# Kernel optimization log

Measured on AMD Instinct MI355X. Metric: run time of the kernel, lower is better.

## Reference

```python
import jax, jax.numpy as jnp
import numpy as np

B, N, E = 2, 2048, 1024
H, D = 16, 64  # context_dim = H*D = 1024


def setup_inputs() -> dict:
    key = jax.random.key(0)
    ks = jax.random.split(key, 6)
    s = 0.02
    return {
        "input_emb": jax.random.normal(ks[0], (B, N, E), dtype=jnp.float32),
        "Wq": jax.random.normal(ks[1], (E, H * D), dtype=jnp.float32) * s,
        "Wk": jax.random.normal(ks[2], (E, D), dtype=jnp.float32) * s,
        "Wv": jax.random.normal(ks[3], (E, D), dtype=jnp.float32) * s,
        "Wo": jax.random.normal(ks[4], (H * D, H * D), dtype=jnp.float32) * s,
        "bo": jax.random.normal(ks[5], (H * D,), dtype=jnp.float32) * s,
    }


def reference(input_emb, Wq, Wk, Wv, Wo, bo):
    b, n, _ = input_emb.shape
    Q = (input_emb @ Wq).reshape(b, n, H, D)          # (B,N,H,D)
    K = input_emb @ Wk                                 # (B,N,D) shared across heads (MQA)
    V = input_emb @ Wv                                 # (B,N,D)
    # scores: (B,H,N,N); mask is applied before scaling in the torch code,
    # but -inf/scale == -inf so mask-then-scale == scale-then-mask.
    scores = jnp.einsum("bnhd,bmd->bhnm", Q, K) / jnp.sqrt(jnp.float32(D))
    causal = jnp.tril(jnp.ones((n, n), dtype=bool))    # True = keep
    scores = jnp.where(causal[None, None], scores, -jnp.inf)
    weights = jax.nn.softmax(scores, axis=-1)          # dropout rate 0.0 -> identity
    Z = jnp.einsum("bhnm,bmd->bnhd", weights, V).reshape(b, n, H * D)
    return Z @ Wo + bo
```

## Files before the change

kernel.cpp:

```cpp
#include <hip/hip_runtime.h>
#include <hip/hip_bf16.h>


#define NQ 2048
#define BATCH 2
#define HEADS 16
#define HD 64
#define EMB 1024
#define NKV 1152

typedef short s16x8 __attribute__((ext_vector_type(8)));
typedef float f32x4 __attribute__((ext_vector_type(4)));
typedef unsigned int u32x4 __attribute__((ext_vector_type(4)));
typedef unsigned short ushort_t;

__device__ __forceinline__ ushort_t f2bf(float f) {
    unsigned u = __builtin_bit_cast(unsigned, f);
    u += 0x7fff + ((u >> 16) & 1);
    return (ushort_t)(u >> 16);
}

__device__ __forceinline__ void store_out(float* p, float v) { *p = v; }
__device__ __forceinline__ void store_out(ushort_t* p, float v) { *p = f2bf(v); }

#define GL16(g, l)                                                                  \
    __builtin_amdgcn_global_load_lds(                                               \
        (const __attribute__((address_space(1))) unsigned int*)(g),                 \
        (__attribute__((address_space(3))) unsigned int*)(l), 16, 0, 0)

__global__ __launch_bounds__(256) void prep(const float* __restrict__ x,
                                            const float* __restrict__ Wq,
                                            const float* __restrict__ Wk,
                                            const float* __restrict__ Wv,
                                            const float* __restrict__ Wo,
                                            ushort_t* __restrict__ xb,
                                            ushort_t* __restrict__ Wqkv_t,
                                            ushort_t* __restrict__ Wo_t) {
    const int bid = blockIdx.x, t = threadIdx.x;
    if (bid < 4096) {
        const int i = bid * 1024 + t * 4;
        const float4 v = *(const float4*)&x[i];
        ushort_t o[4] = {f2bf(v.x), f2bf(v.y), f2bf(v.z), f2bf(v.w)};
        *(uint2*)&xb[i] = *(uint2*)o;
        return;
    }
    int tb = bid - 4096;
    const float* src; ushort_t* dst; int N, n0, k0;
    if (tb < 1024)      { src = Wq; N = 1024; dst = Wqkv_t;
                          n0 = (tb & 31) * 32; k0 = (tb >> 5) * 32; }
    else if (tb < 1088) { tb -= 1024; src = Wk; N = 64; dst = Wqkv_t + (size_t)1024 * EMB;
                          n0 = (tb & 1) * 32; k0 = (tb >> 1) * 32; }
    else if (tb < 1152) { tb -= 1088; src = Wv; N = 64; dst = Wqkv_t + (size_t)1088 * EMB;
                          n0 = (tb & 1) * 32; k0 = (tb >> 1) * 32; }
    else                { tb -= 1152; src = Wo; N = 1024; dst = Wo_t;
                          n0 = (tb & 31) * 32; k0 = (tb >> 5) * 32; }
    __shared__ float tile[32][33];
    const int tx = t & 31, ty = t >> 5;
#pragma unroll
    for (int i = 0; i < 32; i += 8)
        tile[ty + i][tx] = src[(size_t)(k0 + ty + i) * N + n0 + tx];
    __syncthreads();
#pragma unroll
    for (int i = 0; i < 32; i += 8)
        dst[(size_t)(n0 + ty + i) * EMB + k0 + tx] = f2bf(tile[tx][ty + i]);
}

template<bool HAS_BIAS, bool WRITE_VT, typename OutT>
__global__ __launch_bounds__(256) void gemm_bf16(const ushort_t* __restrict__ A,
                                                 const ushort_t* __restrict__ Bt,
                                                 const float* __restrict__ bias,
                                                 OutT* __restrict__ C,
                                                 ushort_t* __restrict__ Vt,
                                                 int M, int N, int K) {
    __shared__ __align__(16) ushort_t Al[64 * 32];
    __shared__ __align__(16) ushort_t Bl[128 * 32];
    const int t = threadIdx.x;
    const int w = t >> 6, lane = t & 63, quad = lane >> 4, ln = lane & 15;
    const int row0 = blockIdx.y * 64, col0 = blockIdx.x * 128;

    const int rA = t >> 2;
    const int lcA = (t & 3) ^ ((rA >> 1) & 3);
    const int rB1 = 64 + rA;
    const ushort_t* ga  = A  + (size_t)(row0 + rA) * K + lcA * 8;
    const ushort_t* gb0 = Bt + (size_t)(col0 + rA) * K + lcA * 8;
    const ushort_t* gb1 = Bt + (size_t)(col0 + rB1) * K + lcA * 8;
    ushort_t* lA  = Al + w * 512;
    ushort_t* lB0 = Bl + w * 512;
    ushort_t* lB1 = Bl + 2048 + w * 512;

    f32x4 acc[4][2] = {};
    const int sw = (ln >> 1) & 3;
    for (int k0 = 0; k0 < K; k0 += 32) {
        GL16(ga, lA); GL16(gb0, lB0); GL16(gb1, lB1);
        ga += 32; gb0 += 32; gb1 += 32;
        __syncthreads();

        s16x8 af[4], bf[2];
#pragma unroll
        for (int mt = 0; mt < 4; ++mt)
            af[mt] = *(const s16x8*)&Al[(mt * 16 + ln) * 32 + ((quad ^ sw) * 8)];
#pragma unroll
        for (int nt = 0; nt < 2; ++nt)
            bf[nt] = *(const s16x8*)&Bl[(w * 32 + nt * 16 + ln) * 32 + ((quad ^ sw) * 8)];
#pragma unroll
        for (int mt = 0; mt < 4; ++mt)
#pragma unroll
            for (int nt = 0; nt < 2; ++nt)
                acc[mt][nt] = __builtin_amdgcn_mfma_f32_16x16x32_bf16(
                    af[mt], bf[nt], acc[mt][nt], 0, 0, 0);
        __syncthreads();
    }

#pragma unroll
    for (int nt = 0; nt < 2; ++nt) {
        const int col = col0 + w * 32 + nt * 16 + ln;
        const float bv = HAS_BIAS ? bias[col] : 0.f;
#pragma unroll
        for (int mt = 0; mt < 4; ++mt) {
#pragma unroll
            for (int r = 0; r < 4; ++r) {
                const int row = row0 + mt * 16 + quad * 4 + r;
                float v = acc[mt][nt][r] + bv;
                if (WRITE_VT && col < 1024) v *= 0.18033688011112043f;
                store_out(&C[(size_t)row * N + col], v);
            }
            if (WRITE_VT && col >= 1088) {
                const int d = col - 1088;
                const int n = row0 + mt * 16 + quad * 4;
                const int bb = n >> 11, nn = n & 2047;
                ushort_t tmp[4] = {f2bf(acc[mt][nt][0]), f2bf(acc[mt][nt][1]),
                                   f2bf(acc[mt][nt][2]), f2bf(acc[mt][nt][3])};
                *(uint2*)&Vt[((size_t)bb * 64 + d) * NQ + nn] = *(uint2*)tmp;
            }
        }
    }
}

__device__ __forceinline__ void stage_tile(ushort_t* lds, const ushort_t* g,
                                           size_t rstride, int w, int lane) {
#pragma unroll
    for (int it = 0; it < 2; ++it) {
        const int u = (w * 2 + it) * 64 + lane;
        const int row = u >> 3, pc = u & 7;
        const int lc = pc ^ (row & 7);
        GL16(g + (size_t)row * rstride + lc * 8, lds + (size_t)(w * 2 + it) * 512);
    }
}

__device__ __forceinline__ void stage_k(ushort_t* lds, const ushort_t* g,
                                        int w, int lane) {
#pragma unroll
    for (int it = 0; it < 2; ++it) {
        const int u = (w * 2 + it) * 64 + lane;
        const int row = u >> 3, pc = u & 7;
        const int lc = pc ^ (row & 7);
        const int grow = (row & 32) | (((row >> 2) & 3) << 3) |
                         (((row >> 4) & 1) << 2) | (row & 3);
        GL16(g + (size_t)grow * NKV + lc * 8, lds + (size_t)(w * 2 + it) * 512);
    }
}

__device__ __forceinline__ s16x8 frag(const ushort_t* lds, int row, int lc) {
    const int phys = lc ^ (row & 7);
    return *(const s16x8*)&lds[row * 64 + phys * 8];
}

__global__ __launch_bounds__(256, 4) void attn_mfma(const ushort_t* __restrict__ QKV,
                                                    const ushort_t* __restrict__ Vt,
                                                    ushort_t* __restrict__ Z) {
    const int bid = blockIdx.x;
    const int b = (bid >> 4) & 1, h = bid & 15;
    const int i = bid >> 5, k = i >> 3, j = i & 7;
    const int qt = (k == 0) ? 2 * j : (k == 1) ? 31 - 2 * j
                 : (k == 2) ? 2 * j + 1 : 30 - 2 * j;
    const int t = threadIdx.x;
    const int w = t >> 6, lane = t & 63, quad = lane >> 4, ln = lane & 15;

    __shared__ __align__(16) ushort_t Kl[2][64 * 64];
    __shared__ __align__(16) ushort_t Vl[2][64 * 64];

    const ushort_t* Kg = QKV + (size_t)b * NQ * NKV + 1024;
    const ushort_t* Vg = Vt + (size_t)b * 64 * NQ;

    const ushort_t* Qg = QKV + (size_t)(b * NQ + qt * 64 + w * 16 + ln) * NKV + h * HD;
    const s16x8 aQ0 = *(const s16x8*)(Qg + quad * 8);
    const s16x8 aQ1 = *(const s16x8*)(Qg + 32 + quad * 8);

    stage_k(Kl[0], Kg, w, lane);
    stage_tile(Vl[0], Vg, NQ, w, lane);
    __syncthreads();

    f32x4 o[4];
#pragma unroll
    for (int ii = 0; ii < 4; ++ii) o[ii] = f32x4{0.f, 0.f, 0.f, 0.f};
    float mrow = -1e30f, lrow = 0.f;
    const int qrel = w * 16 + ln;

#pragma unroll 1
    for (int jt = 0; jt <= qt; ++jt) {
        const int cur = jt & 1;
        if (jt < qt) {
            stage_k(Kl[cur ^ 1], Kg + (size_t)(jt + 1) * 64 * NKV, w, lane);
            stage_tile(Vl[cur ^ 1], Vg + (jt + 1) * 64, NQ, w, lane);
        }
        const ushort_t* Kc = Kl[cur];
        const ushort_t* Vc = Vl[cur];

        f32x4 s[4];
        __builtin_amdgcn_s_setprio(1);
#pragma unroll
        for (int nt = 0; nt < 4; ++nt) {
            f32x4 acc = f32x4{0.f, 0.f, 0.f, 0.f};
            acc = __builtin_amdgcn_mfma_f32_16x16x32_bf16(
                frag(Kc, nt * 16 + ln, quad), aQ0, acc, 0, 0, 0);
            acc = __builtin_amdgcn_mfma_f32_16x16x32_bf16(
                frag(Kc, nt * 16 + ln, 4 + quad), aQ1, acc, 0, 0, 0);
            s[nt] = acc;
        }
        __builtin_amdgcn_s_setprio(0);

        if (jt == qt) {
#pragma unroll
            for (int nt = 0; nt < 4; ++nt)
#pragma unroll
                for (int r = 0; r < 4; ++r) {
                    const int kv = (nt >> 1) * 32 + quad * 8 + (nt & 1) * 4 + r;
                    if (kv > qrel) s[nt][r] = -1e30f;
                }
        }

        float m0 = fmaxf(fmaxf(s[0][0], s[0][1]), fmaxf(s[0][2], s[0][3]));
        float m1 = fmaxf(fmaxf(s[1][0], s[1][1]), fmaxf(s[1][2], s[1][3]));
        float m2 = fmaxf(fmaxf(s[2][0], s[2][1]), fmaxf(s[2][2], s[2][3]));
        float m3 = fmaxf(fmaxf(s[3][0], s[3][1]), fmaxf(s[3][2], s[3][3]));
        float rmax = fmaxf(fmaxf(m0, m1), fmaxf(m2, m3));
        rmax = fmaxf(rmax, __shfl_xor(rmax, 16));
        rmax = fmaxf(rmax, __shfl_xor(rmax, 32));

        if (!__all(rmax - mrow <= 8.f)) {
            const float mnew = fmaxf(mrow, rmax);
            const float al = __builtin_amdgcn_exp2f(mrow - mnew);
            mrow = mnew;
            lrow *= al;
#pragma unroll
            for (int ntd = 0; ntd < 4; ++ntd)
#pragma unroll
                for (int r = 0; r < 4; ++r) o[ntd][r] *= al;
        }

        float rsum = 0.f;
#pragma unroll
        for (int nt = 0; nt < 4; ++nt)
#pragma unroll
            for (int r = 0; r < 4; ++r) {
                const float pv = __builtin_amdgcn_exp2f(s[nt][r] - mrow);
                s[nt][r] = pv;
                rsum += pv;
            }
        rsum += __shfl_xor(rsum, 16);
        rsum += __shfl_xor(rsum, 32);
        lrow += rsum;

        unsigned pw0[4], pw1[4];
#pragma unroll
        for (int jj = 0; jj < 4; ++jj) {
            const int nt0 = jj >> 1, rr = 2 * (jj & 1);
            asm("v_cvt_pk_bf16_f32 %0, %1, %2"
                : "=v"(pw0[jj]) : "v"(s[nt0][rr]), "v"(s[nt0][rr + 1]));
            asm("v_cvt_pk_bf16_f32 %0, %1, %2"
                : "=v"(pw1[jj]) : "v"(s[2 + nt0][rr]), "v"(s[2 + nt0][rr + 1]));
        }
        const u32x4 q0 = {pw0[0], pw0[1], pw0[2], pw0[3]};
        const u32x4 q1 = {pw1[0], pw1[1], pw1[2], pw1[3]};
        const s16x8 bP0 = __builtin_bit_cast(s16x8, q0);
        const s16x8 bP1 = __builtin_bit_cast(s16x8, q1);

        __builtin_amdgcn_s_setprio(1);
#pragma unroll
        for (int ntd = 0; ntd < 4; ++ntd) {
            o[ntd] = __builtin_amdgcn_mfma_f32_16x16x32_bf16(
                frag(Vc, ntd * 16 + ln, quad), bP0, o[ntd], 0, 0, 0);
            o[ntd] = __builtin_amdgcn_mfma_f32_16x16x32_bf16(
                frag(Vc, ntd * 16 + ln, 4 + quad), bP1, o[ntd], 0, 0, 0);
        }
        __builtin_amdgcn_s_setprio(0);
        __syncthreads();
    }

    const float invl = 1.f / lrow;
    const size_t row = (size_t)(b * NQ + qt * 64 + w * 16 + ln);
#pragma unroll
    for (int ntd = 0; ntd < 4; ++ntd) {
        ushort_t tmp[4];
#pragma unroll
        for (int r = 0; r < 4; ++r) tmp[r] = f2bf(o[ntd][r] * invl);
        *(uint2*)&Z[row * EMB + h * HD + ntd * 16 + quad * 4] = *(uint2*)tmp;
    }
}

extern "C" void kernel_launch(void* const* d_in, const int* in_sizes, int n_in,
                              void* d_out, int out_size, void* d_ws, size_t ws_size,
                              hipStream_t stream) {
    const float* x  = (const float*)d_in[0];
    const float* Wq = (const float*)d_in[1];
    const float* Wk = (const float*)d_in[2];
    const float* Wv = (const float*)d_in[3];
    const float* Wo = (const float*)d_in[4];
    const float* bo = (const float*)d_in[5];
    float* out = (float*)d_out;

    const int M = BATCH * NQ;
    char* ws = (char*)d_ws;
    ushort_t* xb     = (ushort_t*)ws;
    ushort_t* Wqkv_t = (ushort_t*)(ws + (size_t)8  * 1024 * 1024);
    ushort_t* Wo_t   = (ushort_t*)(ws + (size_t)11 * 1024 * 1024);
    ushort_t* QKV    = (ushort_t*)(ws + (size_t)13 * 1024 * 1024);
    ushort_t* Vt     = (ushort_t*)(ws + (size_t)23 * 1024 * 1024);
    ushort_t* Zb     = (ushort_t*)(ws + (size_t)24 * 1024 * 1024);

    dim3 blk(256);
    prep<<<dim3(6272), blk, 0, stream>>>(x, Wq, Wk, Wv, Wo, xb, Wqkv_t, Wo_t);
    gemm_bf16<false, true, ushort_t><<<dim3(NKV / 128, M / 64), blk, 0, stream>>>(
        xb, Wqkv_t, nullptr, QKV, Vt, M, NKV, EMB);
    attn_mfma<<<dim3(1024), blk, 0, stream>>>(QKV, Vt, Zb);
    gemm_bf16<true, false, float><<<dim3(EMB / 128, M / 64), blk, 0, stream>>>(
        Zb, Wo_t, bo, out, nullptr, M, EMB, EMB);
}
```

Before: 166.5 us.

## Enlarge GEMM tiles to 128x128x64 with double-buffered LDS and block swizzle

Reworks the bf16 GEMM used for the QKV and output projections. Tiles grow from 64x128 with K-step 32 to 128x128 with K-step 64, and each wave now computes a 64x64 sub-tile. LDS is double-buffered so the global loads for the next K-step are issued before the current step's MFMAs, and the block index is remapped so neighbouring blocks are spread across the grid. The intent is more data reuse per load, fewer barriers per unit of work, and overlap of memory traffic with compute. In exchange it uses 64KB of LDS and more registers per block, and launches half as many blocks (288 and 256), which may underfill the GPU's compute units.

```diff
diff --git a/kernel.cpp b/kernel.cpp
--- a/kernel.cpp
+++ b/kernel.cpp
@@ -65,68 +65,105 @@
         dst[(size_t)(n0 + ty + i) * EMB + k0 + tx] = f2bf(tile[tx][ty + i]);
 }
 
+__device__ __forceinline__ s16x8 frag(const ushort_t* lds, int row, int lc) {
+    const int phys = lc ^ (row & 7);
+    return *(const s16x8*)&lds[row * 64 + phys * 8];
+}
+
 template<bool HAS_BIAS, bool WRITE_VT, typename OutT>
-__global__ __launch_bounds__(256) void gemm_bf16(const ushort_t* __restrict__ A,
-                                                 const ushort_t* __restrict__ Bt,
-                                                 const float* __restrict__ bias,
-                                                 OutT* __restrict__ C,
-                                                 ushort_t* __restrict__ Vt,
-                                                 int M, int N, int K) {
-    __shared__ __align__(16) ushort_t Al[64 * 32];
-    __shared__ __align__(16) ushort_t Bl[128 * 32];
+__global__ __launch_bounds__(256, 2) void gemm_bf16(const ushort_t* __restrict__ A,
+                                                    const ushort_t* __restrict__ Bt,
+                                                    const float* __restrict__ bias,
+                                                    OutT* __restrict__ C,
+                                                    ushort_t* __restrict__ Vt,
+                                                    int M, int N, int K) {
+    __shared__ __align__(16) ushort_t Al[2][128 * 64];
+    __shared__ __align__(16) ushort_t Bl[2][128 * 64];
     const int t = threadIdx.x;
     const int w = t >> 6, lane = t & 63, quad = lane >> 4, ln = lane & 15;
-    const int row0 = blockIdx.y * 64, col0 = blockIdx.x * 128;
-
-    const int rA = t >> 2;
-    const int lcA = (t & 3) ^ ((rA >> 1) & 3);
-    const int rB1 = 64 + rA;
-    const ushort_t* ga  = A  + (size_t)(row0 + rA) * K + lcA * 8;
-    const ushort_t* gb0 = Bt + (size_t)(col0 + rA) * K + lcA * 8;
-    const ushort_t* gb1 = Bt + (size_t)(col0 + rB1) * K + lcA * 8;
-    ushort_t* lA  = Al + w * 512;
-    ushort_t* lB0 = Bl + w * 512;
-    ushort_t* lB1 = Bl + 2048 + w * 512;
-
-    f32x4 acc[4][2] = {};
-    const int sw = (ln >> 1) & 3;
-    for (int k0 = 0; k0 < K; k0 += 32) {
-        GL16(ga, lA); GL16(gb0, lB0); GL16(gb1, lB1);
-        ga += 32; gb0 += 32; gb1 += 32;
+    const int wm = w >> 1, wn = w & 1;
+
+    const int nwg = gridDim.x * gridDim.y;
+    int lin = blockIdx.y * gridDim.x + blockIdx.x;
+    lin = (lin & 7) * (nwg >> 3) + (lin >> 3);
+    const int bx = lin % gridDim.x, by = lin / gridDim.x;
+    const int row0 = by * 128, col0 = bx * 128;
+
+    const ushort_t* pA[4];
+    const ushort_t* pB[4];
+#pragma unroll
+    for (int it = 0; it < 4; ++it) {
+        const int u = (w * 4 + it) * 64 + lane;
+        const int row = u >> 3, pc = u & 7;
+        const int lc = pc ^ (row & 7);
+        pA[it] = A + (size_t)(row0 + row) * K + lc * 8;
+        pB[it] = Bt + (size_t)(col0 + row) * K + lc * 8;
+    }
+
+#define STAGE_AB(la, lb)                                                            \
+    {                                                                               \
+        _Pragma("unroll")                                                           \
+        for (int it = 0; it < 4; ++it) {                                            \
+            GL16(pA[it], (la) + (w * 4 + it) * 512);                                \
+            GL16(pB[it], (lb) + (w * 4 + it) * 512);                                \
+            pA[it] += 64;                                                           \
+            pB[it] += 64;                                                           \
+        }                                                                           \
+    }
+
+    f32x4 acc[4][4] = {};
+    const int nk = K >> 6;
+
+    STAGE_AB(Al[0], Bl[0]);
+    __syncthreads();
+
+#pragma unroll 1
+    for (int ks = 0; ks < nk; ++ks) {
+        const int cur = ks & 1;
+        if (ks + 1 < nk) STAGE_AB(Al[cur ^ 1], Bl[cur ^ 1]);
+
+        const ushort_t* la = Al[cur];
+        const ushort_t* lb = Bl[cur];
+        s16x8 af[4][2], bf[4][2];
+#pragma unroll
+        for (int mt = 0; mt < 4; ++mt) {
+            af[mt][0] = frag(la, wm * 64 + mt * 16 + ln, quad);
+            af[mt][1] = frag(la, wm * 64 + mt * 16 + ln, 4 + quad);
+        }
+#pragma unroll
+        for (int nt = 0; nt < 4; ++nt) {
+            bf[nt][0] = frag(lb, wn * 64 + nt * 16 + ln, quad);
+            bf[nt][1] = frag(lb, wn * 64 + nt * 16 + ln, 4 + quad);
+        }
+#pragma unroll
+        for (int mt = 0; mt < 4; ++mt)
+#pragma unroll
+            for (int nt = 0; nt < 4; ++nt) {
+                acc[mt][nt] = __builtin_amdgcn_mfma_f32_16x16x32_bf16(
+                    af[mt][0], bf[nt][0], acc[mt][nt], 0, 0, 0);
+                acc[mt][nt] = __builtin_amdgcn_mfma_f32_16x16x32_bf16(
+                    af[mt][1], bf[nt][1], acc[mt][nt], 0, 0, 0);
+            }
         __syncthreads();
-
-        s16x8 af[4], bf[2];
-#pragma unroll
-        for (int mt = 0; mt < 4; ++mt)
-            af[mt] = *(const s16x8*)&Al[(mt * 16 + ln) * 32 + ((quad ^ sw) * 8)];
-#pragma unroll
-        for (int nt = 0; nt < 2; ++nt)
-            bf[nt] = *(const s16x8*)&Bl[(w * 32 + nt * 16 + ln) * 32 + ((quad ^ sw) * 8)];
-#pragma unroll
-        for (int mt = 0; mt < 4; ++mt)
-#pragma unroll
-            for (int nt = 0; nt < 2; ++nt)
-                acc[mt][nt] = __builtin_amdgcn_mfma_f32_16x16x32_bf16(
-                    af[mt], bf[nt], acc[mt][nt], 0, 0, 0);
-        __syncthreads();
-    }
-
-#pragma unroll
-    for (int nt = 0; nt < 2; ++nt) {
-        const int col = col0 + w * 32 + nt * 16 + ln;
+    }
+#undef STAGE_AB
+
+#pragma unroll
+    for (int nt = 0; nt < 4; ++nt) {
+        const int col = col0 + wn * 64 + nt * 16 + ln;
         const float bv = HAS_BIAS ? bias[col] : 0.f;
 #pragma unroll
         for (int mt = 0; mt < 4; ++mt) {
 #pragma unroll
             for (int r = 0; r < 4; ++r) {
-                const int row = row0 + mt * 16 + quad * 4 + r;
+                const int row = row0 + wm * 64 + mt * 16 + quad * 4 + r;
                 float v = acc[mt][nt][r] + bv;
                 if (WRITE_VT && col < 1024) v *= 0.18033688011112043f;
                 store_out(&C[(size_t)row * N + col], v);
             }
             if (WRITE_VT && col >= 1088) {
                 const int d = col - 1088;
-                const int n = row0 + mt * 16 + quad * 4;
+                const int n = row0 + wm * 64 + mt * 16 + quad * 4;
                 const int bb = n >> 11, nn = n & 2047;
                 ushort_t tmp[4] = {f2bf(acc[mt][nt][0]), f2bf(acc[mt][nt][1]),
                                    f2bf(acc[mt][nt][2]), f2bf(acc[mt][nt][3])};
@@ -158,11 +195,6 @@
                          (((row >> 4) & 1) << 2) | (row & 3);
         GL16(g + (size_t)grow * NKV + lc * 8, lds + (size_t)(w * 2 + it) * 512);
     }
-}
-
-__device__ __forceinline__ s16x8 frag(const ushort_t* lds, int row, int lc) {
-    const int phys = lc ^ (row & 7);
-    return *(const s16x8*)&lds[row * 64 + phys * 8];
 }
 
 __global__ __launch_bounds__(256, 4) void attn_mfma(const ushort_t* __restrict__ QKV,
@@ -320,9 +352,9 @@
 
     dim3 blk(256);
     prep<<<dim3(6272), blk, 0, stream>>>(x, Wq, Wk, Wv, Wo, xb, Wqkv_t, Wo_t);
-    gemm_bf16<false, true, ushort_t><<<dim3(NKV / 128, M / 64), blk, 0, stream>>>(
+    gemm_bf16<false, true, ushort_t><<<dim3(NKV / 128, M / 64 / 2), blk, 0, stream>>>(
         xb, Wqkv_t, nullptr, QKV, Vt, M, NKV, EMB);
     attn_mfma<<<dim3(1024), blk, 0, stream>>>(QKV, Vt, Zb);
-    gemm_bf16<true, false, float><<<dim3(EMB / 128, M / 64), blk, 0, stream>>>(
+    gemm_bf16<true, false, float><<<dim3(EMB / 128, M / 64 / 2), blk, 0, stream>>>(
         Zb, Wo_t, bo, out, nullptr, M, EMB, EMB);
 }
```

Result: faster. 161.1 us (-3.2%).
